# Kernel tuning notes

Hardware: AMD Instinct MI355X
Metric: run time of the kernel (lower is better)

Reference implementation:

```python
import jax, jax.numpy as jnp
import numpy as np
from jax import lax

BN_EPS = 1e-5


def setup_inputs() -> dict:
    key = jax.random.key(0)
    k1, k2, k3, k4, k5, k6 = jax.random.split(key, 6)
    N, Cin, H, W = 32, 512, 56, 56
    Cout = 32
    Ctot = 1024
    return {
        "x_slice": jax.random.normal(k1, (N, Cin, H, W), dtype=jnp.float32),
        "out_map": jnp.zeros((N, Ctot, H, W), dtype=jnp.float32),
        "bn_weight": jax.random.uniform(k2, (Cin,), dtype=jnp.float32, minval=0.5, maxval=1.5),
        "bn_bias": jax.random.normal(k3, (Cin,), dtype=jnp.float32) * 0.1,
        "running_mean": jax.random.normal(k4, (Cin,), dtype=jnp.float32) * 0.1,
        "running_var": jax.random.uniform(k5, (Cin,), dtype=jnp.float32, minval=0.5, maxval=1.5),
        "conv_weight": jax.random.normal(k6, (Cout, Cin, 3, 3), dtype=jnp.float32) * 0.02,
        "write_offset": 512,
    }


def reference(x_slice, out_map, bn_weight, bn_bias, running_mean, running_var, conv_weight, write_offset):
    # BatchNorm with running stats (inference normalization), fused scale/shift
    inv_std = lax.rsqrt(running_var + BN_EPS)            # [C]
    scale = (bn_weight * inv_std)[None, :, None, None]   # [1,C,1,1]
    shift = (bn_bias - running_mean * bn_weight * inv_std)[None, :, None, None]
    relu_out = jnp.maximum(x_slice * scale + shift, 0.0)  # BN + ReLU fused
    # 3x3 conv, padding=1, no bias (NCHW / OIHW)
    conv_out = lax.conv_general_dilated(
        relu_out, conv_weight,
        window_strides=(1, 1), padding=((1, 1), (1, 1)),
        dimension_numbers=("NCHW", "OIHW", "NCHW"))
    # write into offset slice of the preallocated feature map, return the slice
    out_map = lax.dynamic_update_slice_in_dim(out_map, conv_out, write_offset, axis=1)
    Cout = conv_weight.shape[0]
    return lax.dynamic_slice_in_dim(out_map, write_offset, Cout, axis=1)
```

## Files before the change

### kernel.cpp

```cpp
#include <hip/hip_runtime.h>
#include <cstdint>

#define CIN    512
#define COUT   32
#define IMH    56
#define IMW    56
#define NB     32
#define CHUNKS 16
#define XSTR   40
#define NTH    512
#define YT     7
#define SLOTS  2240
#define SPT    5
#define BUFS   (10 * 58 * XSTR)

typedef __attribute__((ext_vector_type(8))) short v8s;
typedef __attribute__((ext_vector_type(4))) float v4f;

__device__ __forceinline__ unsigned short f2bf(float f) {
    unsigned u = __builtin_bit_cast(unsigned, f);
    u += 0x7FFFu + ((u >> 16) & 1u);
    return (unsigned short)(u >> 16);
}

__global__ void wtransform(const float* __restrict__ cw,
                           const float* __restrict__ bn_w, const float* __restrict__ bn_b,
                           const float* __restrict__ rm,   const float* __restrict__ rv,
                           unsigned short* __restrict__ w2, float4* __restrict__ bq) {
    int idx = blockIdx.x * blockDim.x + threadIdx.x;
    if (idx < 256) {
        int c = idx * 2;
        float s0 = bn_w[c]     * rsqrtf(rv[c]     + 1e-5f);
        float s1 = bn_w[c + 1] * rsqrtf(rv[c + 1] + 1e-5f);
        bq[idx] = make_float4(s0, bn_b[c] - rm[c] * s0, s1, bn_b[c + 1] - rm[c + 1] * s1);
    }
    if (idx >= CHUNKS * 9 * 2 * 64 * 8) return;
    int j    = idx & 7;
    int lane = (idx >> 3) & 63;
    int mt   = (idx >> 9) & 1;
    int tmp  = idx >> 10;
    int tap  = tmp % 9;
    int gc   = tmp / 9;
    int m = mt * 16 + (lane & 15);
    int k = gc * 32 + (lane >> 4) * 8 + j;
    w2[idx] = f2bf(cw[((size_t)m * CIN + k) * 9 + tap]);
}

struct SlotTab {
    int lbase[SPT];
    int gofs[SPT];
    int actm;
};

__device__ __forceinline__ void load_inputs(const float* __restrict__ p0,
                                            const SlotTab& st,
                                            float4 (&va)[SPT], float4 (&vb)[SPT]) {
    #pragma unroll
    for (int j = 0; j < SPT; ++j) {
        if (st.actm & (1 << j)) {
            const float* p = p0 + st.gofs[j];
            va[j] = *(const float4*)p;
            vb[j] = *(const float4*)(p + 3136);
        }
    }
}

__device__ __forceinline__ void pack_chunk(unsigned short* __restrict__ bp,
                                           const SlotTab& st, float4 bn,
                                           const float4 (&va)[SPT], const float4 (&vb)[SPT]) {
    #pragma unroll
    for (int j = 0; j < SPT; ++j) {
        if (st.actm & (1 << j)) {
            float a0 = fmaxf(fmaf(va[j].x, bn.x, bn.y), 0.f);
            float a1 = fmaxf(fmaf(va[j].y, bn.x, bn.y), 0.f);
            float a2 = fmaxf(fmaf(va[j].z, bn.x, bn.y), 0.f);
            float a3 = fmaxf(fmaf(va[j].w, bn.x, bn.y), 0.f);
            float b0 = fmaxf(fmaf(vb[j].x, bn.z, bn.w), 0.f);
            float b1 = fmaxf(fmaf(vb[j].y, bn.z, bn.w), 0.f);
            float b2 = fmaxf(fmaf(vb[j].z, bn.z, bn.w), 0.f);
            float b3 = fmaxf(fmaf(vb[j].w, bn.z, bn.w), 0.f);
            unsigned u0 = (unsigned)f2bf(a0) | ((unsigned)f2bf(b0) << 16);
            unsigned u1 = (unsigned)f2bf(a1) | ((unsigned)f2bf(b1) << 16);
            unsigned u2 = (unsigned)f2bf(a2) | ((unsigned)f2bf(b2) << 16);
            unsigned u3 = (unsigned)f2bf(a3) | ((unsigned)f2bf(b3) << 16);
            int base = st.lbase[j];
            *(unsigned*)&bp[base]            = u0;
            *(unsigned*)&bp[base + XSTR]     = u1;
            *(unsigned*)&bp[base + 2 * XSTR] = u2;
            *(unsigned*)&bp[base + 3 * XSTR] = u3;
        }
    }
}

__device__ __forceinline__ void mfma_chunk(const unsigned short* __restrict__ bp,
                                           const v8s (&aw0)[9], const v8s (&aw1)[9],
                                           const int (&b_base)[4], int ntile,
                                           v4f (&acc)[4][2]) {
    #pragma unroll
    for (int tap = 0; tap < 9; ++tap) {
        const int toff = ((tap / 3) * 58 + (tap % 3)) * XSTR;
        #pragma unroll
        for (int i = 0; i < 4; ++i) {
            if (i < ntile) {
                v8s b = *(const v8s*)&bp[b_base[i] + toff];
                acc[i][0] = __builtin_amdgcn_mfma_f32_16x16x32_bf16(aw0[tap], b, acc[i][0], 0, 0, 0);
                acc[i][1] = __builtin_amdgcn_mfma_f32_16x16x32_bf16(aw1[tap], b, acc[i][1], 0, 0, 0);
            }
        }
    }
}

__device__ __forceinline__ void do_chunk(int gc, const float* __restrict__ xn,
                                         const unsigned short* __restrict__ w2,
                                         const float4* __restrict__ s_bq,
                                         unsigned short* __restrict__ bp,
                                         const SlotTab& st,
                                         float4 (&va)[SPT], float4 (&vb)[SPT],
                                         const int (&b_base)[4], int ntile,
                                         v4f (&acc)[4][2], int c2, int lane,
                                         bool prefetch) {
    v8s aw0[9], aw1[9];
    const v8s* wpv = (const v8s*)(w2 + (size_t)gc * 9216);
    #pragma unroll
    for (int t = 0; t < 9; ++t) {
        aw0[t] = wpv[t * 128 + lane];
        aw1[t] = wpv[t * 128 + 64 + lane];
    }

    float4 bn = s_bq[gc * 16 + c2];

    pack_chunk(bp, st, bn, va, vb);

    if (prefetch)
        load_inputs(xn + (size_t)(gc + 2) * 32 * 3136, st, va, vb);

    asm volatile("s_waitcnt lgkmcnt(0)" ::: "memory");
    __builtin_amdgcn_s_barrier();

    __builtin_amdgcn_s_setprio(1);
    mfma_chunk(bp, aw0, aw1, b_base, ntile, acc);
    __builtin_amdgcn_s_setprio(0);
}

__global__ __launch_bounds__(NTH, 1)
void conv_mfma(const float* __restrict__ x,
               const unsigned short* __restrict__ w2,
               const float4* __restrict__ bq,
               float* __restrict__ out)
{
    __shared__ __align__(16) unsigned short s_x[2][BUFS];
    __shared__ __align__(16) float4 s_bq[CHUNKS * 16];

    const int tid  = threadIdx.x;
    const int lane = tid & 63;
    const int wv   = tid >> 6;
    const int yt   = blockIdx.x;
    const int n    = blockIdx.y;
    const int y0   = yt * 8;
    const int c2   = tid & 15;

    if (tid < CHUNKS * 16) s_bq[tid] = bq[tid];

    SlotTab st;
    st.actm = 0;
    #pragma unroll
    for (int j = 0; j < SPT; ++j) {
        int slot = tid + j * NTH;
        bool inr = (slot < SLOTS);
        int rest = slot >> 4;
        int xg = rest % 14;
        int r  = rest / 14;
        int iy = y0 - 1 + r;
        bool v = inr && (iy >= 0) && (iy < IMH);
        if (v) st.actm |= (1 << j);
        st.lbase[j] = (r * 58 + xg * 4 + 1) * XSTR + c2 * 2;
        st.gofs[j]  = c2 * 2 * 3136 + (v ? iy : 0) * 56 + xg * 4;
    }

    for (int i = tid; i < 2 * 10 * 2 * 20; i += NTH) {
        int kq = i % 20;
        int t  = i / 20;
        int side = t & 1;
        int r  = (t >> 1) % 10;
        int b  = t / 20;
        *(unsigned*)&s_x[b][(r * 58 + (side ? 57 : 0)) * XSTR + kq * 2] = 0u;
    }
    if (yt == 0 || yt == YT - 1) {
        int r = (yt == 0) ? 0 : 9;
        for (int i = tid; i < 2 * 58 * 20; i += NTH) {
            int b = i >= 58 * 20;
            int q = i - b * 58 * 20;
            *(unsigned*)&s_x[b][r * 58 * XSTR + q * 2] = 0u;
        }
    }

    const int ntile = (wv < 4) ? 4 : 3;
    const int tbase = (wv < 4) ? wv * 4 : 16 + (wv - 4) * 3;
    int b_base[4];
    v4f acc[4][2];
    const v4f zero4 = {0.f, 0.f, 0.f, 0.f};
    #pragma unroll
    for (int i = 0; i < 4; ++i) {
        int T  = tbase + ((i < ntile) ? i : 0);
        int p  = T * 16 + (lane & 15);
        int py = p / 56, px = p % 56;
        b_base[i] = (py * 58 + px) * XSTR + (lane >> 4) * 8;
        acc[i][0] = zero4;
        acc[i][1] = zero4;
    }

    const float* xn = x + (size_t)n * CIN * 3136;

    float4 vaA[SPT], vbA[SPT], vaB[SPT], vbB[SPT];
    load_inputs(xn, st, vaA, vbA);
    load_inputs(xn + (size_t)32 * 3136, st, vaB, vbB);

    asm volatile("s_waitcnt lgkmcnt(0)" ::: "memory");
    __builtin_amdgcn_s_barrier();

    for (int gc = 0; gc < CHUNKS; gc += 2) {
        do_chunk(gc,     xn, w2, s_bq, &s_x[0][0], st, vaA, vbA,
                 b_base, ntile, acc, c2, lane, gc + 2 < CHUNKS);
        do_chunk(gc + 1, xn, w2, s_bq, &s_x[1][0], st, vaB, vbB,
                 b_base, ntile, acc, c2, lane, gc + 3 < CHUNKS);
    }

    const int prow = (lane >> 4) * 4;
    #pragma unroll
    for (int i = 0; i < 4; ++i) {
        if (i >= ntile) break;
        int T  = tbase + i;
        int p  = T * 16 + (lane & 15);
        int py = p / 56, px = p % 56;
        size_t o0 = (size_t)n * COUT * 3136 + (size_t)(y0 + py) * 56 + px;
        #pragma unroll
        for (int mt = 0; mt < 2; ++mt) {
            #pragma unroll
            for (int r = 0; r < 4; ++r) {
                int cout = mt * 16 + prow + r;
                out[o0 + (size_t)cout * 3136] = acc[i][mt][r];
            }
        }
    }
}

extern "C" void kernel_launch(void* const* d_in, const int* in_sizes, int n_in,
                              void* d_out, int out_size, void* d_ws, size_t ws_size,
                              hipStream_t stream) {
    const float* x      = (const float*)d_in[0];
    const float* bn_w   = (const float*)d_in[2];
    const float* bn_b   = (const float*)d_in[3];
    const float* r_mean = (const float*)d_in[4];
    const float* r_var  = (const float*)d_in[5];
    const float* cw     = (const float*)d_in[6];
    float* out = (float*)d_out;

    unsigned short* w2 = (unsigned short*)d_ws;
    float4* bq = (float4*)((char*)d_ws + 294912);

    wtransform<<<dim3(576), dim3(256), 0, stream>>>(cw, bn_w, bn_b, r_mean, r_var, w2, bq);

    conv_mfma<<<dim3(YT, NB), dim3(NTH), 0, stream>>>(x, w2, bq, out);
}
```

Before: 78.74 us.

## Remap MFMA pixel tiles to 2x8 blocks with reused B fragments

Changes each wave's pixel tiles from linear 16-pixel runs to 2-row by 8-column blocks stacked vertically, so the last tap row of one tile is reused as the first tap row of the next, cutting LDS reads. This idles the eighth wave during the MFMA phase, where before the load was split 4/3 across waves. It also swaps the manual bf16 rounding for the hardware packed-convert instruction and drops the s_setprio around the MFMA loop. Keeping the saved fragments live adds register pressure.

```diff
diff --git a/kernel.cpp b/kernel.cpp
--- a/kernel.cpp
+++ b/kernel.cpp
@@ -65,6 +65,12 @@
     }
 }
 
+__device__ __forceinline__ unsigned cvtpk(float lo, float hi) {
+    unsigned r;
+    asm("v_cvt_pk_bf16_f32 %0, %1, %2" : "=v"(r) : "v"(lo), "v"(hi));
+    return r;
+}
+
 __device__ __forceinline__ void pack_chunk(unsigned short* __restrict__ bp,
                                            const SlotTab& st, float4 bn,
                                            const float4 (&va)[SPT], const float4 (&vb)[SPT]) {
@@ -79,10 +85,10 @@
             float b1 = fmaxf(fmaf(vb[j].y, bn.z, bn.w), 0.f);
             float b2 = fmaxf(fmaf(vb[j].z, bn.z, bn.w), 0.f);
             float b3 = fmaxf(fmaf(vb[j].w, bn.z, bn.w), 0.f);
-            unsigned u0 = (unsigned)f2bf(a0) | ((unsigned)f2bf(b0) << 16);
-            unsigned u1 = (unsigned)f2bf(a1) | ((unsigned)f2bf(b1) << 16);
-            unsigned u2 = (unsigned)f2bf(a2) | ((unsigned)f2bf(b2) << 16);
-            unsigned u3 = (unsigned)f2bf(a3) | ((unsigned)f2bf(b3) << 16);
+            unsigned u0 = cvtpk(a0, b0);
+            unsigned u1 = cvtpk(a1, b1);
+            unsigned u2 = cvtpk(a2, b2);
+            unsigned u3 = cvtpk(a3, b3);
             int base = st.lbase[j];
             *(unsigned*)&bp[base]            = u0;
             *(unsigned*)&bp[base + XSTR]     = u1;
@@ -94,15 +100,26 @@
 
 __device__ __forceinline__ void mfma_chunk(const unsigned short* __restrict__ bp,
                                            const v8s (&aw0)[9], const v8s (&aw1)[9],
-                                           const int (&b_base)[4], int ntile,
+                                           int pbase, bool active,
                                            v4f (&acc)[4][2]) {
-    #pragma unroll
-    for (int tap = 0; tap < 9; ++tap) {
-        const int toff = ((tap / 3) * 58 + (tap % 3)) * XSTR;
+    if (!active) return;
+    v8s sav0, sav1, sav2;
+    #pragma unroll
+    for (int i = 0; i < 4; ++i) {
         #pragma unroll
-        for (int i = 0; i < 4; ++i) {
-            if (i < ntile) {
-                v8s b = *(const v8s*)&bp[b_base[i] + toff];
+        for (int ty = 0; ty < 3; ++ty) {
+            #pragma unroll
+            for (int tx = 0; tx < 3; ++tx) {
+                v8s b;
+                if (ty == 0 && i > 0) {
+                    b = (tx == 0) ? sav0 : (tx == 1) ? sav1 : sav2;
+                } else {
+                    b = *(const v8s*)&bp[pbase + ((2 * i + ty) * 58 + tx) * XSTR];
+                }
+                if (ty == 2) {
+                    if (tx == 0) sav0 = b; else if (tx == 1) sav1 = b; else sav2 = b;
+                }
+                const int tap = ty * 3 + tx;
                 acc[i][0] = __builtin_amdgcn_mfma_f32_16x16x32_bf16(aw0[tap], b, acc[i][0], 0, 0, 0);
                 acc[i][1] = __builtin_amdgcn_mfma_f32_16x16x32_bf16(aw1[tap], b, acc[i][1], 0, 0, 0);
             }
@@ -116,7 +133,7 @@
                                          unsigned short* __restrict__ bp,
                                          const SlotTab& st,
                                          float4 (&va)[SPT], float4 (&vb)[SPT],
-                                         const int (&b_base)[4], int ntile,
+                                         int pbase, bool active,
                                          v4f (&acc)[4][2], int c2, int lane,
                                          bool prefetch) {
     v8s aw0[9], aw1[9];
@@ -137,9 +154,7 @@
     asm volatile("s_waitcnt lgkmcnt(0)" ::: "memory");
     __builtin_amdgcn_s_barrier();
 
-    __builtin_amdgcn_s_setprio(1);
-    mfma_chunk(bp, aw0, aw1, b_base, ntile, acc);
-    __builtin_amdgcn_s_setprio(0);
+    mfma_chunk(bp, aw0, aw1, pbase, active, acc);
 }
 
 __global__ __launch_bounds__(NTH, 1)
@@ -194,20 +209,14 @@
         }
     }
 
-    const int ntile = (wv < 4) ? 4 : 3;
-    const int tbase = (wv < 4) ? wv * 4 : 16 + (wv - 4) * 3;
-    int b_base[4];
+    const bool active = (wv < 7);
+    const int dy  = (lane & 15) >> 3;
+    const int px8 = lane & 7;
+    const int pbase = (dy * 58 + wv * 8 + px8) * XSTR + (lane >> 4) * 8;
     v4f acc[4][2];
     const v4f zero4 = {0.f, 0.f, 0.f, 0.f};
     #pragma unroll
-    for (int i = 0; i < 4; ++i) {
-        int T  = tbase + ((i < ntile) ? i : 0);
-        int p  = T * 16 + (lane & 15);
-        int py = p / 56, px = p % 56;
-        b_base[i] = (py * 58 + px) * XSTR + (lane >> 4) * 8;
-        acc[i][0] = zero4;
-        acc[i][1] = zero4;
-    }
+    for (int i = 0; i < 4; ++i) { acc[i][0] = zero4; acc[i][1] = zero4; }
 
     const float* xn = x + (size_t)n * CIN * 3136;
 
@@ -220,25 +229,25 @@
 
     for (int gc = 0; gc < CHUNKS; gc += 2) {
         do_chunk(gc,     xn, w2, s_bq, &s_x[0][0], st, vaA, vbA,
-                 b_base, ntile, acc, c2, lane, gc + 2 < CHUNKS);
+                 pbase, active, acc, c2, lane, gc + 2 < CHUNKS);
         do_chunk(gc + 1, xn, w2, s_bq, &s_x[1][0], st, vaB, vbB,
-                 b_base, ntile, acc, c2, lane, gc + 3 < CHUNKS);
-    }
-
-    const int prow = (lane >> 4) * 4;
-    #pragma unroll
-    for (int i = 0; i < 4; ++i) {
-        if (i >= ntile) break;
-        int T  = tbase + i;
-        int p  = T * 16 + (lane & 15);
-        int py = p / 56, px = p % 56;
-        size_t o0 = (size_t)n * COUT * 3136 + (size_t)(y0 + py) * 56 + px;
+                 pbase, active, acc, c2, lane, gc + 3 < CHUNKS);
+    }
+
+    if (active) {
+        const int prow = (lane >> 4) * 4;
         #pragma unroll
-        for (int mt = 0; mt < 2; ++mt) {
+        for (int i = 0; i < 4; ++i) {
+            int py = 2 * i + dy;
+            int px = wv * 8 + px8;
+            size_t o0 = (size_t)n * COUT * 3136 + (size_t)(y0 + py) * 56 + px;
             #pragma unroll
-            for (int r = 0; r < 4; ++r) {
-                int cout = mt * 16 + prow + r;
-                out[o0 + (size_t)cout * 3136] = acc[i][mt][r];
+            for (int mt = 0; mt < 2; ++mt) {
+                #pragma unroll
+                for (int r = 0; r < 4; ++r) {
+                    int cout = mt * 16 + prow + r;
+                    out[o0 + (size_t)cout * 3136] = acc[i][mt][r];
+                }
             }
         }
     }
```

Measured after the change: 72.87 us. -7.5%, faster.
